# Kernel tuning notes

Measured on AMD Instinct MI355X. Metric: run time of the kernel, lower is better.

The kernel has to match this reference:

```python
import jax, jax.numpy as jnp
import numpy as np

N = 100000   # nodes
E = 1600000  # edges
D = 128      # input feature dim
H = 128      # hidden dim
C = 40       # output classes


def _gcn_conv(x, W, b, src, dst, norm):
    # PyG GCNConv: h = x @ W; out_i = sum_j (d_i^-1/2 d_j^-1/2) h_j over in-edges,
    # including self-loops, then + bias. norm = deg^-1/2 with self-loop-augmented degree.
    h = x @ W                                    # [N, H]
    coef = norm[src] * norm[dst]                 # [E]
    agg = jax.ops.segment_sum(h[src] * coef[:, None], dst, num_segments=N)
    agg = agg + h * (norm * norm)[:, None]       # self-loop term
    return agg + b


def setup_inputs() -> dict:
    key = jax.random.key(0)
    ks = jax.random.split(key, 12)
    x = jax.random.normal(ks[0], (N, D), dtype=jnp.float32)
    edge_index = jax.random.randint(ks[1], (2, E), 0, N, dtype=jnp.int64)

    def lin(k, fan_in, fan_out):
        s = 1.0 / np.sqrt(fan_in)
        return jax.random.uniform(k, (fan_in, fan_out), jnp.float32, -s, s)

    return {
        "x": x,
        "edge_index": edge_index,
        "W1": lin(ks[2], D, H), "b1": jnp.zeros((H,), jnp.float32),
        "W2": lin(ks[3], H, H), "b2": jnp.zeros((H,), jnp.float32),
        "W3": lin(ks[4], H, H), "b3": jnp.zeros((H,), jnp.float32),
        "Wp1": lin(ks[5], H, H), "bp1": jnp.zeros((H,), jnp.float32),
        "Wp2": lin(ks[6], H, C), "bp2": jnp.zeros((C,), jnp.float32),
    }


def reference(x, edge_index, W1, b1, W2, b2, W3, b3, Wp1, bp1, Wp2, bp2):
    src, dst = edge_index[0], edge_index[1]
    # degree with self-loops (GCNConv adds self-loops by default)
    deg = jax.ops.segment_sum(jnp.ones((E,), jnp.float32), dst, num_segments=N) + 1.0
    norm = jax.lax.rsqrt(deg)                    # deg^-1/2

    h = x
    for W, b in ((W1, b1), (W2, b2), (W3, b3)):
        h = _gcn_conv(h, W, b, src, dst, norm)
        h = jax.nn.relu(h)
        # dropout is a no-op at inference / rate 0

    h = h @ Wp1 + bp1
    h = h @ Wp2 + bp2
    return jax.nn.log_softmax(h, axis=1)
```

## Files before the change

### kernel.cpp

```cpp
#include <hip/hip_runtime.h>
#include <hip/hip_bf16.h>
#include <math.h>


#define DH 128
#define NC 40
#define BN 256
#define MAXNB 512
#define CH 8192
#define ECAP 6144
#define SP 136

typedef __attribute__((ext_vector_type(8))) short bf16x8;
typedef __attribute__((ext_vector_type(4))) float f32x4;

__device__ __forceinline__ unsigned short f2bf(float f) {
    unsigned u = __float_as_uint(f);
    unsigned r = (u + 0x7fffu + ((u >> 16) & 1u)) >> 16;
    return (unsigned short)r;
}
__device__ __forceinline__ unsigned pack2(float lo, float hi) {
    return (unsigned)f2bf(lo) | ((unsigned)f2bf(hi) << 16);
}


__global__ __launch_bounds__(256) void bucket_hist(const int* __restrict__ dst, int E,
                                                   unsigned* __restrict__ bcnt) {
    __shared__ unsigned h[MAXNB];
    int tid = threadIdx.x;
    for (int i = tid; i < MAXNB; i += 256) h[i] = 0;
    __syncthreads();
    int e0 = blockIdx.x * CH;
    int e1 = min(e0 + CH, E);
    for (int i = e0 + tid; i < e1; i += 256)
        atomicAdd(&h[dst[i] >> 8], 1u);
    __syncthreads();
    for (int i = tid; i < MAXNB; i += 256)
        if (h[i]) atomicAdd(&bcnt[i], h[i]);
}

__global__ __launch_bounds__(256) void bucket_alloc(const unsigned* __restrict__ bcnt,
                                                    unsigned* __restrict__ bbase,
                                                    unsigned* __restrict__ bpos,
                                                    unsigned* __restrict__ cursor, int NB) {
    int i = blockIdx.x * 256 + threadIdx.x;
    if (i < NB) {
        unsigned c = bcnt[i];
        unsigned o = atomicAdd(cursor, c);
        bbase[i] = o;
        bpos[i] = o;
    }
}

__global__ __launch_bounds__(256) void bucket_scatter(const int* __restrict__ src,
                                                      const int* __restrict__ dst, int E,
                                                      unsigned* __restrict__ bpos,
                                                      unsigned* __restrict__ ebuf) {
    __shared__ unsigned hist[MAXNB];
    __shared__ unsigned lbase[MAXNB];
    __shared__ unsigned gbase[MAXNB];
    __shared__ unsigned cur[MAXNB];
    __shared__ unsigned sorted[CH];
    __shared__ unsigned short sbkt[CH];
    __shared__ unsigned total;

    int tid = threadIdx.x;
    int e0 = blockIdx.x * CH;
    int nE = min(CH, E - e0);

    for (int i = tid; i < MAXNB; i += 256) { hist[i] = 0; cur[i] = 0; }
    if (tid == 0) total = 0;
    __syncthreads();

    for (int i = tid; i < nE; i += 256)
        atomicAdd(&hist[dst[e0 + i] >> 8], 1u);
    __syncthreads();

    for (int i = tid; i < MAXNB; i += 256) {
        unsigned h = hist[i];
        lbase[i] = h ? atomicAdd(&total, h) : 0u;
        gbase[i] = h ? atomicAdd(&bpos[i], h) : 0u;
    }
    __syncthreads();

    for (int i = tid; i < nE; i += 256) {
        int s = src[e0 + i];
        int d = dst[e0 + i];
        unsigned b = (unsigned)d >> 8;
        unsigned r = atomicAdd(&cur[b], 1u);
        unsigned p = lbase[b] + r;
        sorted[p] = ((unsigned)s << 8) | ((unsigned)d & 255u);
        sbkt[p] = (unsigned short)b;
    }
    __syncthreads();

    for (int p = tid; p < nE; p += 256) {
        unsigned b = sbkt[p];
        ebuf[gbase[b] + (p - lbase[b])] = sorted[p];
    }
}

__global__ __launch_bounds__(256) void bucket_csr(const unsigned* __restrict__ ebuf,
                                                  const unsigned* __restrict__ bbase,
                                                  const unsigned* __restrict__ bcnt,
                                                  unsigned* __restrict__ off,
                                                  unsigned* __restrict__ cnt,
                                                  float* __restrict__ nrm,
                                                  int* __restrict__ csr, int N) {
    __shared__ unsigned h[BN];
    __shared__ unsigned nb[BN];
    __shared__ unsigned ncur[BN];
    __shared__ int lcsr[ECAP];
    __shared__ unsigned tot;

    int b = blockIdx.x;
    int tid = threadIdx.x;
    unsigned ebase = bbase[b];
    unsigned ecnt = bcnt[b];

    h[tid] = 0;
    if (tid == 0) tot = 0;
    __syncthreads();

    for (unsigned i = tid; i < ecnt; i += 256)
        atomicAdd(&h[ebuf[ebase + i] & 255u], 1u);
    __syncthreads();

    unsigned myh = h[tid];
    unsigned mybase = myh ? atomicAdd(&tot, myh) : 0u;
    nb[tid] = mybase;
    ncur[tid] = 0;
    int node = b * BN + tid;
    if (node < N) {
        off[node] = ebase + mybase;
        cnt[node] = myh;
        nrm[node] = rsqrtf((float)myh + 1.0f);
    }
    __syncthreads();

    if (ecnt <= ECAP) {
        for (unsigned i = tid; i < ecnt; i += 256) {
            unsigned v = ebuf[ebase + i];
            unsigned nl = v & 255u;
            unsigned r = atomicAdd(&ncur[nl], 1u);
            lcsr[nb[nl] + r] = (int)(v >> 8);
        }
        __syncthreads();
        for (unsigned i = tid; i < ecnt; i += 256)
            csr[ebase + i] = lcsr[i];
    } else {
        for (unsigned i = tid; i < ecnt; i += 256) {
            unsigned v = ebuf[ebase + i];
            unsigned nl = v & 255u;
            unsigned r = atomicAdd(&ncur[nl], 1u);
            csr[ebase + nb[nl] + r] = (int)(v >> 8);
        }
    }
}


__global__ __launch_bounds__(256) void prep_w(const float* __restrict__ W1,
                                              const float* __restrict__ W2,
                                              const float* __restrict__ W3,
                                              const float* __restrict__ Wp1,
                                              const float* __restrict__ bp1,
                                              const float* __restrict__ Wp2,
                                              const float* __restrict__ bp2,
                                              unsigned short* __restrict__ Wt,
                                              unsigned short* __restrict__ Wft,
                                              float* __restrict__ bfh) {
    int id = blockIdx.x * 256 + threadIdx.x;
    if (id < 3 * DH * DH) {
        int l = id >> 14, r = id & (DH * DH - 1);
        int k = r >> 7, n = r & 127;
        const float* W = (l == 0) ? W1 : (l == 1) ? W2 : W3;
        Wt[l * DH * DH + n * DH + k] = f2bf(W[k * DH + n]);
    } else if (id < 3 * DH * DH + 48 * DH) {
        int o = id - 3 * DH * DH;
        int c = o >> 7, k = o & 127;
        float acc = 0.f;
        if (c < NC)
            for (int j = 0; j < DH; ++j) acc += Wp1[k * DH + j] * Wp2[j * NC + c];
        Wft[c * DH + k] = f2bf(acc);
    } else if (id < 3 * DH * DH + 48 * DH + 48) {
        int c = id - 3 * DH * DH - 48 * DH;
        float acc = 0.f;
        if (c < NC) {
            acc = bp2[c];
            for (int j = 0; j < DH; ++j) acc += bp1[j] * Wp2[j * NC + c];
        }
        bfh[c] = acc;
    }
}


__global__ __launch_bounds__(256) void gemm_mfma_f32(const float* __restrict__ X,
                                                     const unsigned short* __restrict__ Wt,
                                                     const float* __restrict__ nrm,
                                                     unsigned short* __restrict__ outb,
                                                     int nrows) {
    const int tid = threadIdx.x;
    const int wave = tid >> 6;
    const int lane = tid & 63;
    const int m = lane & 15;
    const int quad = lane >> 4;
    const int rbase = blockIdx.x * 128 + wave * 32;

    union U8 { bf16x8 v; unsigned u[4]; };

    f32x4 acc[2][8];
#pragma unroll
    for (int rt = 0; rt < 2; ++rt)
#pragma unroll
        for (int ct = 0; ct < 8; ++ct) acc[rt][ct] = (f32x4){0.f, 0.f, 0.f, 0.f};

#pragma unroll
    for (int kt = 0; kt < 4; ++kt) {
        const int kof = kt * 32 + quad * 8;
        bf16x8 a[2], b[8];
#pragma unroll
        for (int rt = 0; rt < 2; ++rt) {
            int r = rbase + rt * 16 + m;
            r = (r < nrows) ? r : (nrows - 1);
            const float* p = X + (size_t)r * DH + kof;
            float4 u0 = *(const float4*)p;
            float4 u1 = *(const float4*)(p + 4);
            U8 t;
            t.u[0] = pack2(u0.x, u0.y);
            t.u[1] = pack2(u0.z, u0.w);
            t.u[2] = pack2(u1.x, u1.y);
            t.u[3] = pack2(u1.z, u1.w);
            a[rt] = t.v;
        }
#pragma unroll
        for (int ct = 0; ct < 8; ++ct)
            b[ct] = *(const bf16x8*)(Wt + (ct * 16 + m) * DH + kof);
#pragma unroll
        for (int rt = 0; rt < 2; ++rt)
#pragma unroll
            for (int ct = 0; ct < 8; ++ct)
                acc[rt][ct] = __builtin_amdgcn_mfma_f32_16x16x32_bf16(a[rt], b[ct], acc[rt][ct], 0, 0, 0);
    }

#pragma unroll
    for (int rt = 0; rt < 2; ++rt)
#pragma unroll
        for (int reg = 0; reg < 4; ++reg) {
            int r = rbase + rt * 16 + quad * 4 + reg;
            if (r < nrows) {
                float s = nrm[r];
#pragma unroll
                for (int ct = 0; ct < 8; ++ct)
                    outb[(size_t)r * DH + ct * 16 + m] = f2bf(acc[rt][ct][reg] * s);
            }
        }
}


__device__ __forceinline__ void bf8_add(float* acc, uint4 v) {
    acc[0] += __uint_as_float(v.x << 16);
    acc[1] += __uint_as_float(v.x & 0xffff0000u);
    acc[2] += __uint_as_float(v.y << 16);
    acc[3] += __uint_as_float(v.y & 0xffff0000u);
    acc[4] += __uint_as_float(v.z << 16);
    acc[5] += __uint_as_float(v.z & 0xffff0000u);
    acc[6] += __uint_as_float(v.w << 16);
    acc[7] += __uint_as_float(v.w & 0xffff0000u);
}

__device__ __forceinline__ void gather_phase(const uint4* __restrict__ Abf,
                                             const int* __restrict__ csr,
                                             const unsigned* __restrict__ off,
                                             const unsigned* __restrict__ cnt,
                                             const float* __restrict__ nrm,
                                             const float* __restrict__ bias,
                                             unsigned short (*sA)[SP], int N) {
    const int tid = threadIdx.x;
    const int g = tid >> 4;
    const int lane = tid & 15;
    const int node = blockIdx.x * 16 + g;
    if (node < N) {
        float acc[8];
        {
            uint4 v = Abf[(size_t)node * 16 + lane];
            acc[0] = __uint_as_float(v.x << 16);
            acc[1] = __uint_as_float(v.x & 0xffff0000u);
            acc[2] = __uint_as_float(v.y << 16);
            acc[3] = __uint_as_float(v.y & 0xffff0000u);
            acc[4] = __uint_as_float(v.z << 16);
            acc[5] = __uint_as_float(v.z & 0xffff0000u);
            acc[6] = __uint_as_float(v.w << 16);
            acc[7] = __uint_as_float(v.w & 0xffff0000u);
        }
        unsigned o = off[node];
        unsigned d = cnt[node];

        unsigned e = 0;
        for (; e + 4 <= d; e += 4) {
            int s0 = csr[o + e + 0];
            int s1 = csr[o + e + 1];
            int s2 = csr[o + e + 2];
            int s3 = csr[o + e + 3];
            uint4 v0 = Abf[(size_t)s0 * 16 + lane];
            uint4 v1 = Abf[(size_t)s1 * 16 + lane];
            uint4 v2 = Abf[(size_t)s2 * 16 + lane];
            uint4 v3 = Abf[(size_t)s3 * 16 + lane];
            bf8_add(acc, v0);
            bf8_add(acc, v1);
            bf8_add(acc, v2);
            bf8_add(acc, v3);
        }
        for (; e < d; ++e) {
            int s = csr[o + e];
            uint4 v = Abf[(size_t)s * 16 + lane];
            bf8_add(acc, v);
        }

        float nm = nrm[node];
        float4 b0 = *(const float4*)(bias + lane * 8);
        float4 b1 = *(const float4*)(bias + lane * 8 + 4);
        unsigned short* p = &sA[g][lane * 8];
        p[0] = f2bf(fmaxf(acc[0] * nm + b0.x, 0.f));
        p[1] = f2bf(fmaxf(acc[1] * nm + b0.y, 0.f));
        p[2] = f2bf(fmaxf(acc[2] * nm + b0.z, 0.f));
        p[3] = f2bf(fmaxf(acc[3] * nm + b0.w, 0.f));
        p[4] = f2bf(fmaxf(acc[4] * nm + b1.x, 0.f));
        p[5] = f2bf(fmaxf(acc[5] * nm + b1.y, 0.f));
        p[6] = f2bf(fmaxf(acc[6] * nm + b1.z, 0.f));
        p[7] = f2bf(fmaxf(acc[7] * nm + b1.w, 0.f));
    }
    __syncthreads();
}


__global__ __launch_bounds__(256) void agg_gemm(const uint4* __restrict__ Abf,
                                                const int* __restrict__ csr,
                                                const unsigned* __restrict__ off,
                                                const unsigned* __restrict__ cnt,
                                                const float* __restrict__ nrm,
                                                const float* __restrict__ bias,
                                                const unsigned short* __restrict__ Wt,
                                                unsigned short* __restrict__ outb, int N) {
    __shared__ unsigned short sA[16][SP];
    gather_phase(Abf, csr, off, cnt, nrm, bias, sA, N);

    const int tid = threadIdx.x;
    const int wave = tid >> 6;
    const int l64 = tid & 63;
    const int m = l64 & 15;
    const int quad = l64 >> 4;

    f32x4 acc[2];
    acc[0] = (f32x4){0.f, 0.f, 0.f, 0.f};
    acc[1] = (f32x4){0.f, 0.f, 0.f, 0.f};

#pragma unroll
    for (int kt = 0; kt < 4; ++kt) {
        const int kof = kt * 32 + quad * 8;
        bf16x8 a = *(const bf16x8*)&sA[m][kof];
#pragma unroll
        for (int c2 = 0; c2 < 2; ++c2) {
            const int ct = wave * 2 + c2;
            bf16x8 b = *(const bf16x8*)(Wt + (ct * 16 + m) * DH + kof);
            acc[c2] = __builtin_amdgcn_mfma_f32_16x16x32_bf16(a, b, acc[c2], 0, 0, 0);
        }
    }

#pragma unroll
    for (int reg = 0; reg < 4; ++reg) {
        int r = blockIdx.x * 16 + quad * 4 + reg;
        if (r < N) {
            float s = nrm[r];
#pragma unroll
            for (int c2 = 0; c2 < 2; ++c2)
                outb[(size_t)r * DH + (wave * 2 + c2) * 16 + m] = f2bf(acc[c2][reg] * s);
        }
    }
}


__global__ __launch_bounds__(256) void agg_head(const uint4* __restrict__ Abf,
                                                const int* __restrict__ csr,
                                                const unsigned* __restrict__ off,
                                                const unsigned* __restrict__ cnt,
                                                const float* __restrict__ nrm,
                                                const float* __restrict__ bias,
                                                const unsigned short* __restrict__ Wft,
                                                const float* __restrict__ bfh,
                                                float* __restrict__ out, int N) {
    __shared__ unsigned short sA[16][SP];
    gather_phase(Abf, csr, off, cnt, nrm, bias, sA, N);

    const int tid = threadIdx.x;
    if (tid >= 64) return;
    const int m = tid & 15;
    const int quad = tid >> 4;

    f32x4 acc[3];
#pragma unroll
    for (int ct = 0; ct < 3; ++ct) acc[ct] = (f32x4){0.f, 0.f, 0.f, 0.f};

#pragma unroll
    for (int kt = 0; kt < 4; ++kt) {
        const int kof = kt * 32 + quad * 8;
        bf16x8 a = *(const bf16x8*)&sA[m][kof];
#pragma unroll
        for (int ct = 0; ct < 3; ++ct) {
            bf16x8 b = *(const bf16x8*)(Wft + (ct * 16 + m) * DH + kof);
            acc[ct] = __builtin_amdgcn_mfma_f32_16x16x32_bf16(a, b, acc[ct], 0, 0, 0);
        }
    }

    float bias0 = bfh[m];
    float bias1 = bfh[16 + m];
    float bias2 = bfh[32 + m];

#pragma unroll
    for (int reg = 0; reg < 4; ++reg) {
        float v0 = acc[0][reg] + bias0;
        float v1 = acc[1][reg] + bias1;
        float v2 = (m < 8) ? (acc[2][reg] + bias2) : -1e30f;
        float mx = fmaxf(fmaxf(v0, v1), v2);
#pragma unroll
        for (int dlt = 1; dlt < 16; dlt <<= 1) mx = fmaxf(mx, __shfl_xor(mx, dlt));
        float s = __expf(v0 - mx) + __expf(v1 - mx) + ((m < 8) ? __expf(v2 - mx) : 0.f);
#pragma unroll
        for (int dlt = 1; dlt < 16; dlt <<= 1) s += __shfl_xor(s, dlt);
        float ls = mx + __logf(s);
        int r = blockIdx.x * 16 + quad * 4 + reg;
        if (r < N) {
            out[(size_t)r * NC + m] = v0 - ls;
            out[(size_t)r * NC + 16 + m] = v1 - ls;
            if (m < 8) out[(size_t)r * NC + 32 + m] = v2 - ls;
        }
    }
}


extern "C" void kernel_launch(void* const* d_in, const int* in_sizes, int n_in,
                              void* d_out, int out_size, void* d_ws, size_t ws_size,
                              hipStream_t stream) {
    const float* x   = (const float*)d_in[0];
    const int*   ei  = (const int*)d_in[1];
    const float* W1  = (const float*)d_in[2];
    const float* b1  = (const float*)d_in[3];
    const float* W2  = (const float*)d_in[4];
    const float* b2  = (const float*)d_in[5];
    const float* W3  = (const float*)d_in[6];
    const float* b3  = (const float*)d_in[7];
    const float* Wp1 = (const float*)d_in[8];
    const float* bp1 = (const float*)d_in[9];
    const float* Wp2 = (const float*)d_in[10];
    const float* bp2 = (const float*)d_in[11];
    float* out = (float*)d_out;

    const int N = in_sizes[0] / DH;
    const int E = in_sizes[1] / 2;
    const int* src = ei;
    const int* dst = ei + E;
    const int NB = (N + BN - 1) / BN;

    char* w = (char*)d_ws;
    unsigned short* Ab  = (unsigned short*)w; w += (size_t)N * DH * 2;
    unsigned short* Bb  = (unsigned short*)w; w += (size_t)N * DH * 2;
    int*      csr    = (int*)w;      w += (size_t)E * 4;
    unsigned* ebuf   = (unsigned*)w; w += (size_t)E * 4;
    unsigned* bcnt   = (unsigned*)w; w += MAXNB * 4;
    unsigned* cursor = (unsigned*)w; w += 16;
    unsigned* bbase  = (unsigned*)w; w += MAXNB * 4;
    unsigned* bpos   = (unsigned*)w; w += MAXNB * 4;
    unsigned* off    = (unsigned*)w; w += (size_t)N * 4;
    unsigned* cnt    = (unsigned*)w; w += (size_t)N * 4;
    float*    nrm    = (float*)w;    w += (size_t)N * 4;
    unsigned short* Wt  = (unsigned short*)w; w += 3 * DH * DH * 2;
    unsigned short* Wft = (unsigned short*)w; w += 48 * DH * 2;
    float*    bfh    = (float*)w;    w += 64 * 4;

    const int gC = (E + CH - 1) / CH;

    hipMemsetAsync(bcnt, 0, MAXNB * 4 + 16, stream);
    bucket_hist   <<<gC, 256, 0, stream>>>(dst, E, bcnt);
    bucket_alloc  <<<(NB + 255) / 256, 256, 0, stream>>>(bcnt, bbase, bpos, cursor, NB);
    bucket_scatter<<<gC, 256, 0, stream>>>(src, dst, E, bpos, ebuf);
    bucket_csr    <<<NB, 256, 0, stream>>>(ebuf, bbase, bcnt, off, cnt, nrm, csr, N);
    prep_w<<<(3 * DH * DH + 48 * DH + 48 + 255) / 256, 256, 0, stream>>>(
        W1, W2, W3, Wp1, bp1, Wp2, bp2, Wt, Wft, bfh);

    const int gG = (N + 127) / 128;
    const int gF = (N + 15) / 16;

    gemm_mfma_f32<<<gG, 256, 0, stream>>>(x, Wt, nrm, Ab, N);
    agg_gemm<<<gF, 256, 0, stream>>>((const uint4*)Ab, csr, off, cnt, nrm, b1,
                                     Wt + DH * DH, Bb, N);
    agg_gemm<<<gF, 256, 0, stream>>>((const uint4*)Bb, csr, off, cnt, nrm, b2,
                                     Wt + 2 * DH * DH, Ab, N);
    agg_head<<<gF, 256, 0, stream>>>((const uint4*)Ab, csr, off, cnt, nrm, b3,
                                     Wft, bfh, out, N);
}
```

Measured before the change: 418.0 us.

## Split each node's neighbor gather across two half-groups and use 512-thread blocks

The fused aggregate+GEMM kernels now give each node 32 threads instead of 16. The two halves each sum half of the in-edges and combine through a cross-lane shuffle, which doubles the memory-level parallelism of the irregular gather. Blocks grow to 512 threads, so each of the eight waves now computes one 16-column MFMA tile instead of two. The edge-bucketing chunk size CH also shrinks, giving more blocks in the histogram and scatter kernels. The cost is extra threads per block, shuffle work, and more idle lanes for low-degree nodes.

```diff
diff --git a/kernel.cpp b/kernel.cpp
--- a/kernel.cpp
+++ b/kernel.cpp
@@ -7,7 +7,7 @@
 #define NC 40
 #define BN 256
 #define MAXNB 512
-#define CH 8192
+#define CH 2048
 #define ECAP 6144
 #define SP 136
 
@@ -276,12 +276,18 @@
                                              const float* __restrict__ bias,
                                              unsigned short (*sA)[SP], int N) {
     const int tid = threadIdx.x;
-    const int g = tid >> 4;
-    const int lane = tid & 15;
+    const int g = tid >> 5;
+    const int l32 = tid & 31;
+    const int half = l32 >> 4;
+    const int lane = l32 & 15;
     const int node = blockIdx.x * 16 + g;
+
     if (node < N) {
         float acc[8];
-        {
+        unsigned o = off[node];
+        unsigned d = cnt[node];
+
+        if (half == 0) {
             uint4 v = Abf[(size_t)node * 16 + lane];
             acc[0] = __uint_as_float(v.x << 16);
             acc[1] = __uint_as_float(v.x & 0xffff0000u);
@@ -291,12 +297,14 @@
             acc[5] = __uint_as_float(v.z & 0xffff0000u);
             acc[6] = __uint_as_float(v.w << 16);
             acc[7] = __uint_as_float(v.w & 0xffff0000u);
-        }
-        unsigned o = off[node];
-        unsigned d = cnt[node];
-
-        unsigned e = 0;
-        for (; e + 4 <= d; e += 4) {
+        } else {
+#pragma unroll
+            for (int c = 0; c < 8; ++c) acc[c] = 0.f;
+        }
+
+        unsigned e  = (d * (unsigned)half) >> 1;
+        unsigned e1 = (d * (unsigned)(half + 1)) >> 1;
+        for (; e + 4 <= e1; e += 4) {
             int s0 = csr[o + e + 0];
             int s1 = csr[o + e + 1];
             int s2 = csr[o + e + 2];
@@ -310,30 +318,35 @@
             bf8_add(acc, v2);
             bf8_add(acc, v3);
         }
-        for (; e < d; ++e) {
+        for (; e < e1; ++e) {
             int s = csr[o + e];
             uint4 v = Abf[(size_t)s * 16 + lane];
             bf8_add(acc, v);
         }
 
-        float nm = nrm[node];
-        float4 b0 = *(const float4*)(bias + lane * 8);
-        float4 b1 = *(const float4*)(bias + lane * 8 + 4);
-        unsigned short* p = &sA[g][lane * 8];
-        p[0] = f2bf(fmaxf(acc[0] * nm + b0.x, 0.f));
-        p[1] = f2bf(fmaxf(acc[1] * nm + b0.y, 0.f));
-        p[2] = f2bf(fmaxf(acc[2] * nm + b0.z, 0.f));
-        p[3] = f2bf(fmaxf(acc[3] * nm + b0.w, 0.f));
-        p[4] = f2bf(fmaxf(acc[4] * nm + b1.x, 0.f));
-        p[5] = f2bf(fmaxf(acc[5] * nm + b1.y, 0.f));
-        p[6] = f2bf(fmaxf(acc[6] * nm + b1.z, 0.f));
-        p[7] = f2bf(fmaxf(acc[7] * nm + b1.w, 0.f));
-    }
-    __syncthreads();
-}
-
-
-__global__ __launch_bounds__(256) void agg_gemm(const uint4* __restrict__ Abf,
+#pragma unroll
+        for (int c = 0; c < 8; ++c) acc[c] += __shfl_xor(acc[c], 16);
+
+        if (half == 0) {
+            float nm = nrm[node];
+            float4 b0 = *(const float4*)(bias + lane * 8);
+            float4 b1 = *(const float4*)(bias + lane * 8 + 4);
+            unsigned short* p = &sA[g][lane * 8];
+            p[0] = f2bf(fmaxf(acc[0] * nm + b0.x, 0.f));
+            p[1] = f2bf(fmaxf(acc[1] * nm + b0.y, 0.f));
+            p[2] = f2bf(fmaxf(acc[2] * nm + b0.z, 0.f));
+            p[3] = f2bf(fmaxf(acc[3] * nm + b0.w, 0.f));
+            p[4] = f2bf(fmaxf(acc[4] * nm + b1.x, 0.f));
+            p[5] = f2bf(fmaxf(acc[5] * nm + b1.y, 0.f));
+            p[6] = f2bf(fmaxf(acc[6] * nm + b1.z, 0.f));
+            p[7] = f2bf(fmaxf(acc[7] * nm + b1.w, 0.f));
+        }
+    }
+    __syncthreads();
+}
+
+
+__global__ __launch_bounds__(512) void agg_gemm(const uint4* __restrict__ Abf,
                                                 const int* __restrict__ csr,
                                                 const unsigned* __restrict__ off,
                                                 const unsigned* __restrict__ cnt,
@@ -350,36 +363,25 @@
     const int m = l64 & 15;
     const int quad = l64 >> 4;
 
-    f32x4 acc[2];
-    acc[0] = (f32x4){0.f, 0.f, 0.f, 0.f};
-    acc[1] = (f32x4){0.f, 0.f, 0.f, 0.f};
-
+    f32x4 acc = (f32x4){0.f, 0.f, 0.f, 0.f};
 #pragma unroll
     for (int kt = 0; kt < 4; ++kt) {
         const int kof = kt * 32 + quad * 8;
         bf16x8 a = *(const bf16x8*)&sA[m][kof];
-#pragma unroll
-        for (int c2 = 0; c2 < 2; ++c2) {
-            const int ct = wave * 2 + c2;
-            bf16x8 b = *(const bf16x8*)(Wt + (ct * 16 + m) * DH + kof);
-            acc[c2] = __builtin_amdgcn_mfma_f32_16x16x32_bf16(a, b, acc[c2], 0, 0, 0);
-        }
+        bf16x8 b = *(const bf16x8*)(Wt + (wave * 16 + m) * DH + kof);
+        acc = __builtin_amdgcn_mfma_f32_16x16x32_bf16(a, b, acc, 0, 0, 0);
     }
 
 #pragma unroll
     for (int reg = 0; reg < 4; ++reg) {
         int r = blockIdx.x * 16 + quad * 4 + reg;
-        if (r < N) {
-            float s = nrm[r];
-#pragma unroll
-            for (int c2 = 0; c2 < 2; ++c2)
-                outb[(size_t)r * DH + (wave * 2 + c2) * 16 + m] = f2bf(acc[c2][reg] * s);
-        }
-    }
-}
-
-
-__global__ __launch_bounds__(256) void agg_head(const uint4* __restrict__ Abf,
+        if (r < N)
+            outb[(size_t)r * DH + wave * 16 + m] = f2bf(acc[reg] * nrm[r]);
+    }
+}
+
+
+__global__ __launch_bounds__(512) void agg_head(const uint4* __restrict__ Abf,
                                                 const int* __restrict__ csr,
                                                 const unsigned* __restrict__ off,
                                                 const unsigned* __restrict__ cnt,
@@ -490,10 +492,10 @@
     const int gF = (N + 15) / 16;
 
     gemm_mfma_f32<<<gG, 256, 0, stream>>>(x, Wt, nrm, Ab, N);
-    agg_gemm<<<gF, 256, 0, stream>>>((const uint4*)Ab, csr, off, cnt, nrm, b1,
+    agg_gemm<<<gF, 512, 0, stream>>>((const uint4*)Ab, csr, off, cnt, nrm, b1,
                                      Wt + DH * DH, Bb, N);
-    agg_gemm<<<gF, 256, 0, stream>>>((const uint4*)Bb, csr, off, cnt, nrm, b2,
+    agg_gemm<<<gF, 512, 0, stream>>>((const uint4*)Bb, csr, off, cnt, nrm, b2,
                                      Wt + 2 * DH * DH, Ab, N);
-    agg_head<<<gF, 256, 0, stream>>>((const uint4*)Ab, csr, off, cnt, nrm, b3,
+    agg_head<<<gF, 512, 0, stream>>>((const uint4*)Ab, csr, off, cnt, nrm, b3,
                                      Wft, bfh, out, N);
 }
```

Result: slower. 444.5 us (+6.3%).

## Give each wave its own 16 nodes for gather and GEMM, dropping block sync

Applied to the files above, without the earlier changes.

The fused aggregate+GEMM kernels now assign 16 nodes to each wave rather than 16 nodes to a whole block. Within a wave, all 64 lanes gather one node's row at a time, each lane loading a 4-byte bf16 pair, with an 8-way unrolled edge loop. Each wave then runs the full 128-column MFMA on its own shared tile, so the block-wide __syncthreads goes away and all four waves do MMA work. The trade-off is that nodes are processed serially within a wave, and each gather issues narrower loads, which may reduce memory-level parallelism per lane.

```diff
diff --git a/kernel.cpp b/kernel.cpp
--- a/kernel.cpp
+++ b/kernel.cpp
@@ -257,83 +257,70 @@
 }
 
 
-__device__ __forceinline__ void bf8_add(float* acc, uint4 v) {
-    acc[0] += __uint_as_float(v.x << 16);
-    acc[1] += __uint_as_float(v.x & 0xffff0000u);
-    acc[2] += __uint_as_float(v.y << 16);
-    acc[3] += __uint_as_float(v.y & 0xffff0000u);
-    acc[4] += __uint_as_float(v.z << 16);
-    acc[5] += __uint_as_float(v.z & 0xffff0000u);
-    acc[6] += __uint_as_float(v.w << 16);
-    acc[7] += __uint_as_float(v.w & 0xffff0000u);
-}
-
-__device__ __forceinline__ void gather_phase(const uint4* __restrict__ Abf,
-                                             const int* __restrict__ csr,
-                                             const unsigned* __restrict__ off,
-                                             const unsigned* __restrict__ cnt,
-                                             const float* __restrict__ nrm,
-                                             const float* __restrict__ bias,
-                                             unsigned short (*sA)[SP], int N) {
-    const int tid = threadIdx.x;
-    const int g = tid >> 4;
-    const int lane = tid & 15;
-    const int node = blockIdx.x * 16 + g;
-    if (node < N) {
-        float acc[8];
-        {
-            uint4 v = Abf[(size_t)node * 16 + lane];
-            acc[0] = __uint_as_float(v.x << 16);
-            acc[1] = __uint_as_float(v.x & 0xffff0000u);
-            acc[2] = __uint_as_float(v.y << 16);
-            acc[3] = __uint_as_float(v.y & 0xffff0000u);
-            acc[4] = __uint_as_float(v.z << 16);
-            acc[5] = __uint_as_float(v.z & 0xffff0000u);
-            acc[6] = __uint_as_float(v.w << 16);
-            acc[7] = __uint_as_float(v.w & 0xffff0000u);
-        }
+__device__ __forceinline__ void gather16(const unsigned* __restrict__ Abf,
+                                         const int* __restrict__ csr,
+                                         const unsigned* __restrict__ off,
+                                         const unsigned* __restrict__ cnt,
+                                         const float* __restrict__ nrm,
+                                         const float* __restrict__ bias,
+                                         unsigned short (*sA)[SP], int nb, int N) {
+    const int l = threadIdx.x & 63;
+    const float b0 = bias[l * 2];
+    const float b1 = bias[l * 2 + 1];
+
+    for (int g = 0; g < 16; ++g) {
+        int node = nb + g;
+        if (node >= N) break;
         unsigned o = off[node];
         unsigned d = cnt[node];
 
+        unsigned v = Abf[(size_t)node * 64 + l];
+        float a0 = __uint_as_float(v << 16);
+        float a1 = __uint_as_float(v & 0xffff0000u);
+
         unsigned e = 0;
-        for (; e + 4 <= d; e += 4) {
+        for (; e + 8 <= d; e += 8) {
             int s0 = csr[o + e + 0];
             int s1 = csr[o + e + 1];
             int s2 = csr[o + e + 2];
             int s3 = csr[o + e + 3];
-            uint4 v0 = Abf[(size_t)s0 * 16 + lane];
-            uint4 v1 = Abf[(size_t)s1 * 16 + lane];
-            uint4 v2 = Abf[(size_t)s2 * 16 + lane];
-            uint4 v3 = Abf[(size_t)s3 * 16 + lane];
-            bf8_add(acc, v0);
-            bf8_add(acc, v1);
-            bf8_add(acc, v2);
-            bf8_add(acc, v3);
+            int s4 = csr[o + e + 4];
+            int s5 = csr[o + e + 5];
+            int s6 = csr[o + e + 6];
+            int s7 = csr[o + e + 7];
+            unsigned v0 = Abf[(size_t)s0 * 64 + l];
+            unsigned v1 = Abf[(size_t)s1 * 64 + l];
+            unsigned v2 = Abf[(size_t)s2 * 64 + l];
+            unsigned v3 = Abf[(size_t)s3 * 64 + l];
+            unsigned v4 = Abf[(size_t)s4 * 64 + l];
+            unsigned v5 = Abf[(size_t)s5 * 64 + l];
+            unsigned v6 = Abf[(size_t)s6 * 64 + l];
+            unsigned v7 = Abf[(size_t)s7 * 64 + l];
+            a0 += __uint_as_float(v0 << 16); a1 += __uint_as_float(v0 & 0xffff0000u);
+            a0 += __uint_as_float(v1 << 16); a1 += __uint_as_float(v1 & 0xffff0000u);
+            a0 += __uint_as_float(v2 << 16); a1 += __uint_as_float(v2 & 0xffff0000u);
+            a0 += __uint_as_float(v3 << 16); a1 += __uint_as_float(v3 & 0xffff0000u);
+            a0 += __uint_as_float(v4 << 16); a1 += __uint_as_float(v4 & 0xffff0000u);
+            a0 += __uint_as_float(v5 << 16); a1 += __uint_as_float(v5 & 0xffff0000u);
+            a0 += __uint_as_float(v6 << 16); a1 += __uint_as_float(v6 & 0xffff0000u);
+            a0 += __uint_as_float(v7 << 16); a1 += __uint_as_float(v7 & 0xffff0000u);
         }
         for (; e < d; ++e) {
             int s = csr[o + e];
-            uint4 v = Abf[(size_t)s * 16 + lane];
-            bf8_add(acc, v);
+            unsigned vv = Abf[(size_t)s * 64 + l];
+            a0 += __uint_as_float(vv << 16);
+            a1 += __uint_as_float(vv & 0xffff0000u);
         }
 
         float nm = nrm[node];
-        float4 b0 = *(const float4*)(bias + lane * 8);
-        float4 b1 = *(const float4*)(bias + lane * 8 + 4);
-        unsigned short* p = &sA[g][lane * 8];
-        p[0] = f2bf(fmaxf(acc[0] * nm + b0.x, 0.f));
-        p[1] = f2bf(fmaxf(acc[1] * nm + b0.y, 0.f));
-        p[2] = f2bf(fmaxf(acc[2] * nm + b0.z, 0.f));
-        p[3] = f2bf(fmaxf(acc[3] * nm + b0.w, 0.f));
-        p[4] = f2bf(fmaxf(acc[4] * nm + b1.x, 0.f));
-        p[5] = f2bf(fmaxf(acc[5] * nm + b1.y, 0.f));
-        p[6] = f2bf(fmaxf(acc[6] * nm + b1.z, 0.f));
-        p[7] = f2bf(fmaxf(acc[7] * nm + b1.w, 0.f));
-    }
-    __syncthreads();
-}
-
-
-__global__ __launch_bounds__(256) void agg_gemm(const uint4* __restrict__ Abf,
+        float r0 = fmaxf(a0 * nm + b0, 0.f);
+        float r1 = fmaxf(a1 * nm + b1, 0.f);
+        ((unsigned*)&sA[g][0])[l] = pack2(r0, r1);
+    }
+}
+
+
+__global__ __launch_bounds__(256) void agg_gemm(const unsigned* __restrict__ Abf,
                                                 const int* __restrict__ csr,
                                                 const unsigned* __restrict__ off,
                                                 const unsigned* __restrict__ cnt,
@@ -341,45 +328,41 @@
                                                 const float* __restrict__ bias,
                                                 const unsigned short* __restrict__ Wt,
                                                 unsigned short* __restrict__ outb, int N) {
-    __shared__ unsigned short sA[16][SP];
-    gather_phase(Abf, csr, off, cnt, nrm, bias, sA, N);
-
-    const int tid = threadIdx.x;
-    const int wave = tid >> 6;
-    const int l64 = tid & 63;
+    __shared__ unsigned short sA[4][16][SP];
+    const int wave = threadIdx.x >> 6;
+    const int nb = blockIdx.x * 64 + wave * 16;
+    if (nb >= N) return;
+
+    gather16(Abf, csr, off, cnt, nrm, bias, sA[wave], nb, N);
+
+    const int l64 = threadIdx.x & 63;
     const int m = l64 & 15;
     const int quad = l64 >> 4;
 
-    f32x4 acc[2];
-    acc[0] = (f32x4){0.f, 0.f, 0.f, 0.f};
-    acc[1] = (f32x4){0.f, 0.f, 0.f, 0.f};
-
-#pragma unroll
-    for (int kt = 0; kt < 4; ++kt) {
-        const int kof = kt * 32 + quad * 8;
-        bf16x8 a = *(const bf16x8*)&sA[m][kof];
-#pragma unroll
-        for (int c2 = 0; c2 < 2; ++c2) {
-            const int ct = wave * 2 + c2;
-            bf16x8 b = *(const bf16x8*)(Wt + (ct * 16 + m) * DH + kof);
-            acc[c2] = __builtin_amdgcn_mfma_f32_16x16x32_bf16(a, b, acc[c2], 0, 0, 0);
-        }
-    }
-
-#pragma unroll
-    for (int reg = 0; reg < 4; ++reg) {
-        int r = blockIdx.x * 16 + quad * 4 + reg;
-        if (r < N) {
-            float s = nrm[r];
-#pragma unroll
-            for (int c2 = 0; c2 < 2; ++c2)
-                outb[(size_t)r * DH + (wave * 2 + c2) * 16 + m] = f2bf(acc[c2][reg] * s);
-        }
-    }
-}
-
-
-__global__ __launch_bounds__(256) void agg_head(const uint4* __restrict__ Abf,
+    bf16x8 a[4];
+#pragma unroll
+    for (int kt = 0; kt < 4; ++kt)
+        a[kt] = *(const bf16x8*)&sA[wave][m][kt * 32 + quad * 8];
+
+#pragma unroll
+    for (int ct = 0; ct < 8; ++ct) {
+        f32x4 acc = (f32x4){0.f, 0.f, 0.f, 0.f};
+#pragma unroll
+        for (int kt = 0; kt < 4; ++kt) {
+            bf16x8 b = *(const bf16x8*)(Wt + (ct * 16 + m) * DH + kt * 32 + quad * 8);
+            acc = __builtin_amdgcn_mfma_f32_16x16x32_bf16(a[kt], b, acc, 0, 0, 0);
+        }
+#pragma unroll
+        for (int reg = 0; reg < 4; ++reg) {
+            int r = nb + quad * 4 + reg;
+            if (r < N)
+                outb[(size_t)r * DH + ct * 16 + m] = f2bf(acc[reg] * nrm[r]);
+        }
+    }
+}
+
+
+__global__ __launch_bounds__(256) void agg_head(const unsigned* __restrict__ Abf,
                                                 const int* __restrict__ csr,
                                                 const unsigned* __restrict__ off,
                                                 const unsigned* __restrict__ cnt,
@@ -388,26 +371,30 @@
                                                 const unsigned short* __restrict__ Wft,
                                                 const float* __restrict__ bfh,
                                                 float* __restrict__ out, int N) {
-    __shared__ unsigned short sA[16][SP];
-    gather_phase(Abf, csr, off, cnt, nrm, bias, sA, N);
-
-    const int tid = threadIdx.x;
-    if (tid >= 64) return;
-    const int m = tid & 15;
-    const int quad = tid >> 4;
+    __shared__ unsigned short sA[4][16][SP];
+    const int wave = threadIdx.x >> 6;
+    const int nb = blockIdx.x * 64 + wave * 16;
+    if (nb >= N) return;
+
+    gather16(Abf, csr, off, cnt, nrm, bias, sA[wave], nb, N);
+
+    const int l64 = threadIdx.x & 63;
+    const int m = l64 & 15;
+    const int quad = l64 >> 4;
+
+    bf16x8 a[4];
+#pragma unroll
+    for (int kt = 0; kt < 4; ++kt)
+        a[kt] = *(const bf16x8*)&sA[wave][m][kt * 32 + quad * 8];
 
     f32x4 acc[3];
 #pragma unroll
-    for (int ct = 0; ct < 3; ++ct) acc[ct] = (f32x4){0.f, 0.f, 0.f, 0.f};
-
-#pragma unroll
-    for (int kt = 0; kt < 4; ++kt) {
-        const int kof = kt * 32 + quad * 8;
-        bf16x8 a = *(const bf16x8*)&sA[m][kof];
-#pragma unroll
-        for (int ct = 0; ct < 3; ++ct) {
-            bf16x8 b = *(const bf16x8*)(Wft + (ct * 16 + m) * DH + kof);
-            acc[ct] = __builtin_amdgcn_mfma_f32_16x16x32_bf16(a, b, acc[ct], 0, 0, 0);
+    for (int ct = 0; ct < 3; ++ct) {
+        acc[ct] = (f32x4){0.f, 0.f, 0.f, 0.f};
+#pragma unroll
+        for (int kt = 0; kt < 4; ++kt) {
+            bf16x8 b = *(const bf16x8*)(Wft + (ct * 16 + m) * DH + kt * 32 + quad * 8);
+            acc[ct] = __builtin_amdgcn_mfma_f32_16x16x32_bf16(a[kt], b, acc[ct], 0, 0, 0);
         }
     }
 
@@ -427,7 +414,7 @@
 #pragma unroll
         for (int dlt = 1; dlt < 16; dlt <<= 1) s += __shfl_xor(s, dlt);
         float ls = mx + __logf(s);
-        int r = blockIdx.x * 16 + quad * 4 + reg;
+        int r = nb + quad * 4 + reg;
         if (r < N) {
             out[(size_t)r * NC + m] = v0 - ls;
             out[(size_t)r * NC + 16 + m] = v1 - ls;
@@ -487,13 +474,13 @@
         W1, W2, W3, Wp1, bp1, Wp2, bp2, Wt, Wft, bfh);
 
     const int gG = (N + 127) / 128;
-    const int gF = (N + 15) / 16;
+    const int gF = (N + 63) / 64;
 
     gemm_mfma_f32<<<gG, 256, 0, stream>>>(x, Wt, nrm, Ab, N);
-    agg_gemm<<<gF, 256, 0, stream>>>((const uint4*)Ab, csr, off, cnt, nrm, b1,
+    agg_gemm<<<gF, 256, 0, stream>>>((const unsigned*)Ab, csr, off, cnt, nrm, b1,
                                      Wt + DH * DH, Bb, N);
-    agg_gemm<<<gF, 256, 0, stream>>>((const uint4*)Bb, csr, off, cnt, nrm, b2,
+    agg_gemm<<<gF, 256, 0, stream>>>((const unsigned*)Bb, csr, off, cnt, nrm, b2,
                                      Wt + 2 * DH * DH, Ab, N);
-    agg_head<<<gF, 256, 0, stream>>>((const uint4*)Ab, csr, off, cnt, nrm, b3,
+    agg_head<<<gF, 256, 0, stream>>>((const unsigned*)Ab, csr, off, cnt, nrm, b3,
                                      Wft, bfh, out, N);
 }
```

New measurement: 498.1 us. 19.2% more time.

## Make gather+GEMM wave-independent with per-wave 16-node tiles, dropping block barrier

Applied to the files above, without the earlier changes.

Each wave now gathers its own 16 nodes (four nodes sequentially per 16-lane group) into a private shared-memory tile, then runs the full 128-column MFMA for those rows itself. This removes the block-wide __syncthreads between the gather and the GEMM, and in the head kernel lets all four waves do useful MFMA work instead of one. Each block now covers 64 nodes. The trade-off is less gather parallelism per node, with serial neighbor loops per lane group, and each wave reading the whole weight matrix.

```diff
diff --git a/kernel.cpp b/kernel.cpp
--- a/kernel.cpp
+++ b/kernel.cpp
@@ -268,18 +268,25 @@
     acc[7] += __uint_as_float(v.w & 0xffff0000u);
 }
 
-__device__ __forceinline__ void gather_phase(const uint4* __restrict__ Abf,
-                                             const int* __restrict__ csr,
-                                             const unsigned* __restrict__ off,
-                                             const unsigned* __restrict__ cnt,
-                                             const float* __restrict__ nrm,
-                                             const float* __restrict__ bias,
-                                             unsigned short (*sA)[SP], int N) {
-    const int tid = threadIdx.x;
-    const int g = tid >> 4;
-    const int lane = tid & 15;
-    const int node = blockIdx.x * 16 + g;
-    if (node < N) {
+__device__ __forceinline__ void gather_w4(const uint4* __restrict__ Abf,
+                                          const int* __restrict__ csr,
+                                          const unsigned* __restrict__ off,
+                                          const unsigned* __restrict__ cnt,
+                                          const float* __restrict__ nrm,
+                                          const float* __restrict__ bias,
+                                          unsigned short (*sA)[SP], int nb, int N) {
+    const int l64 = threadIdx.x & 63;
+    const int grp = l64 >> 4;
+    const int lane = l64 & 15;
+    const float4 b0 = *(const float4*)(bias + lane * 8);
+    const float4 b1 = *(const float4*)(bias + lane * 8 + 4);
+
+#pragma unroll
+    for (int j = 0; j < 4; ++j) {
+        const int g = grp * 4 + j;
+        const int node = nb + g;
+        if (node >= N) break;
+
         float acc[8];
         {
             uint4 v = Abf[(size_t)node * 16 + lane];
@@ -317,8 +324,6 @@
         }
 
         float nm = nrm[node];
-        float4 b0 = *(const float4*)(bias + lane * 8);
-        float4 b1 = *(const float4*)(bias + lane * 8 + 4);
         unsigned short* p = &sA[g][lane * 8];
         p[0] = f2bf(fmaxf(acc[0] * nm + b0.x, 0.f));
         p[1] = f2bf(fmaxf(acc[1] * nm + b0.y, 0.f));
@@ -329,7 +334,6 @@
         p[6] = f2bf(fmaxf(acc[6] * nm + b1.z, 0.f));
         p[7] = f2bf(fmaxf(acc[7] * nm + b1.w, 0.f));
     }
-    __syncthreads();
 }
 
 
@@ -341,39 +345,35 @@
                                                 const float* __restrict__ bias,
                                                 const unsigned short* __restrict__ Wt,
                                                 unsigned short* __restrict__ outb, int N) {
-    __shared__ unsigned short sA[16][SP];
-    gather_phase(Abf, csr, off, cnt, nrm, bias, sA, N);
-
-    const int tid = threadIdx.x;
-    const int wave = tid >> 6;
-    const int l64 = tid & 63;
+    __shared__ unsigned short sA[4][16][SP];
+    const int wave = threadIdx.x >> 6;
+    const int nb = blockIdx.x * 64 + wave * 16;
+    if (nb >= N) return;
+
+    gather_w4(Abf, csr, off, cnt, nrm, bias, sA[wave], nb, N);
+
+    const int l64 = threadIdx.x & 63;
     const int m = l64 & 15;
     const int quad = l64 >> 4;
 
-    f32x4 acc[2];
-    acc[0] = (f32x4){0.f, 0.f, 0.f, 0.f};
-    acc[1] = (f32x4){0.f, 0.f, 0.f, 0.f};
-
-#pragma unroll
-    for (int kt = 0; kt < 4; ++kt) {
-        const int kof = kt * 32 + quad * 8;
-        bf16x8 a = *(const bf16x8*)&sA[m][kof];
-#pragma unroll
-        for (int c2 = 0; c2 < 2; ++c2) {
-            const int ct = wave * 2 + c2;
-            bf16x8 b = *(const bf16x8*)(Wt + (ct * 16 + m) * DH + kof);
-            acc[c2] = __builtin_amdgcn_mfma_f32_16x16x32_bf16(a, b, acc[c2], 0, 0, 0);
-        }
-    }
-
-#pragma unroll
-    for (int reg = 0; reg < 4; ++reg) {
-        int r = blockIdx.x * 16 + quad * 4 + reg;
-        if (r < N) {
-            float s = nrm[r];
-#pragma unroll
-            for (int c2 = 0; c2 < 2; ++c2)
-                outb[(size_t)r * DH + (wave * 2 + c2) * 16 + m] = f2bf(acc[c2][reg] * s);
+    bf16x8 a[4];
+#pragma unroll
+    for (int kt = 0; kt < 4; ++kt)
+        a[kt] = *(const bf16x8*)&sA[wave][m][kt * 32 + quad * 8];
+
+#pragma unroll
+    for (int ct = 0; ct < 8; ++ct) {
+        f32x4 acc = (f32x4){0.f, 0.f, 0.f, 0.f};
+#pragma unroll
+        for (int kt = 0; kt < 4; ++kt) {
+            bf16x8 b = *(const bf16x8*)(Wt + (ct * 16 + m) * DH + kt * 32 + quad * 8);
+            acc = __builtin_amdgcn_mfma_f32_16x16x32_bf16(a[kt], b, acc, 0, 0, 0);
+        }
+#pragma unroll
+        for (int reg = 0; reg < 4; ++reg) {
+            int r = nb + quad * 4 + reg;
+            if (r < N)
+                outb[(size_t)r * DH + ct * 16 + m] = f2bf(acc[reg] * nrm[r]);
         }
     }
 }
@@ -388,26 +388,30 @@
                                                 const unsigned short* __restrict__ Wft,
                                                 const float* __restrict__ bfh,
                                                 float* __restrict__ out, int N) {
-    __shared__ unsigned short sA[16][SP];
-    gather_phase(Abf, csr, off, cnt, nrm, bias, sA, N);
-
-    const int tid = threadIdx.x;
-    if (tid >= 64) return;
-    const int m = tid & 15;
-    const int quad = tid >> 4;
+    __shared__ unsigned short sA[4][16][SP];
+    const int wave = threadIdx.x >> 6;
+    const int nb = blockIdx.x * 64 + wave * 16;
+    if (nb >= N) return;
+
+    gather_w4(Abf, csr, off, cnt, nrm, bias, sA[wave], nb, N);
+
+    const int l64 = threadIdx.x & 63;
+    const int m = l64 & 15;
+    const int quad = l64 >> 4;
+
+    bf16x8 a[4];
+#pragma unroll
+    for (int kt = 0; kt < 4; ++kt)
+        a[kt] = *(const bf16x8*)&sA[wave][m][kt * 32 + quad * 8];
 
     f32x4 acc[3];
 #pragma unroll
-    for (int ct = 0; ct < 3; ++ct) acc[ct] = (f32x4){0.f, 0.f, 0.f, 0.f};
-
-#pragma unroll
-    for (int kt = 0; kt < 4; ++kt) {
-        const int kof = kt * 32 + quad * 8;
-        bf16x8 a = *(const bf16x8*)&sA[m][kof];
-#pragma unroll
-        for (int ct = 0; ct < 3; ++ct) {
-            bf16x8 b = *(const bf16x8*)(Wft + (ct * 16 + m) * DH + kof);
-            acc[ct] = __builtin_amdgcn_mfma_f32_16x16x32_bf16(a, b, acc[ct], 0, 0, 0);
+    for (int ct = 0; ct < 3; ++ct) {
+        acc[ct] = (f32x4){0.f, 0.f, 0.f, 0.f};
+#pragma unroll
+        for (int kt = 0; kt < 4; ++kt) {
+            bf16x8 b = *(const bf16x8*)(Wft + (ct * 16 + m) * DH + kt * 32 + quad * 8);
+            acc[ct] = __builtin_amdgcn_mfma_f32_16x16x32_bf16(a[kt], b, acc[ct], 0, 0, 0);
         }
     }
 
@@ -427,7 +431,7 @@
 #pragma unroll
         for (int dlt = 1; dlt < 16; dlt <<= 1) s += __shfl_xor(s, dlt);
         float ls = mx + __logf(s);
-        int r = blockIdx.x * 16 + quad * 4 + reg;
+        int r = nb + quad * 4 + reg;
         if (r < N) {
             out[(size_t)r * NC + m] = v0 - ls;
             out[(size_t)r * NC + 16 + m] = v1 - ls;
@@ -487,7 +491,7 @@
         W1, W2, W3, Wp1, bp1, Wp2, bp2, Wt, Wft, bfh);
 
     const int gG = (N + 127) / 128;
-    const int gF = (N + 15) / 16;
+    const int gF = (N + 63) / 64;
 
     gemm_mfma_f32<<<gG, 256, 0, stream>>>(x, Wt, nrm, Ab, N);
     agg_gemm<<<gF, 256, 0, stream>>>((const uint4*)Ab, csr, off, cnt, nrm, b1,
```

Result: slower. 454.1 us (+8.6%).
